# Kernel optimization log

Measured on AMD Instinct MI355X. Metric: run time of the kernel, lower is better.

## Reference

```python
import jax, jax.numpy as jnp
import numpy as np

B, T, D, H = 4, 2048, 1024, 16
HD = D // H
EPS = 1e-5


def gelu_tanh(x):
    c = jnp.sqrt(jnp.asarray(2.0 / jnp.pi, x.dtype))
    return 0.5 * x * (1.0 + jnp.tanh(c * (x + 0.044715 * x * x * x)))


def layernorm(x, gamma, beta):
    mean = jnp.mean(x, axis=-1, keepdims=True)
    var = jnp.var(x, axis=-1, keepdims=True)
    return gamma * (x - mean) / jnp.sqrt(var + EPS) + beta


def setup_inputs() -> dict:
    key = jax.random.key(0)
    ks = jax.random.split(key, 12)
    s = 0.02
    return {
        "x": jax.random.normal(ks[0], (B, T, D), jnp.float32),
        "Wq": jax.random.normal(ks[1], (D, D), jnp.float32) * s,
        "Wk": jax.random.normal(ks[2], (D, D), jnp.float32) * s,
        "Wv": jax.random.normal(ks[3], (D, D), jnp.float32) * s,
        "Wo": jax.random.normal(ks[4], (D, D), jnp.float32) * s,
        "bo": jnp.zeros((D,), jnp.float32),
        "W1": jax.random.normal(ks[5], (D, 4 * D), jnp.float32) * s,
        "b1": jnp.zeros((4 * D,), jnp.float32),
        "W2": jax.random.normal(ks[6], (4 * D, D), jnp.float32) * s,
        "b2": jnp.zeros((D,), jnp.float32),
        "gamma1": jnp.ones((D,), jnp.float32),
        "beta1": jnp.zeros((D,), jnp.float32),
        "gamma2": jnp.ones((D,), jnp.float32),
        "beta2": jnp.zeros((D,), jnp.float32),
    }


def reference(x, Wq, Wk, Wv, Wo, bo, W1, b1, W2, b2, gamma1, beta1, gamma2, beta2):
    # --- attention sublayer (pre-norm, causal) ---
    h = layernorm(x, gamma1, beta1)
    q = (h @ Wq).reshape(B, T, H, HD).transpose(0, 2, 1, 3)  # (B,H,T,hd)
    k = (h @ Wk).reshape(B, T, H, HD).transpose(0, 2, 1, 3)
    v = (h @ Wv).reshape(B, T, H, HD).transpose(0, 2, 1, 3)
    scores = jnp.einsum("bhqd,bhkd->bhqk", q, k) * (HD ** -0.5)
    causal = jnp.tril(jnp.ones((T, T), bool))
    scores = jnp.where(causal, scores, -jnp.inf)
    w = jax.nn.softmax(scores, axis=-1)
    attn = jnp.einsum("bhqk,bhkd->bhqd", w, v).transpose(0, 2, 1, 3).reshape(B, T, D)
    x = x + (attn @ Wo + bo)
    # --- FFN sublayer ---
    h2 = layernorm(x, gamma2, beta2)
    ff = gelu_tanh(h2 @ W1 + b1) @ W2 + b2
    return x + ff
```

## Files before the change

### kernel.cpp

```cpp
#include <hip/hip_runtime.h>
#include <hip/hip_bf16.h>


typedef __bf16 bf16;
typedef __attribute__((ext_vector_type(8))) __bf16 bf16x8;
typedef __attribute__((ext_vector_type(4))) __bf16 bf16x4;
typedef __attribute__((ext_vector_type(4))) float floatx4;

#define EXPC 0.18033688011112042f

__device__ __forceinline__ void async_cp16(const bf16* g, bf16* l) {
  __builtin_amdgcn_global_load_lds(
      (const __attribute__((address_space(1))) void*)g,
      (__attribute__((address_space(3))) void*)l, 16, 0, 0);
}

__global__ __launch_bounds__(256) void transpose_cvt4(
    const float* __restrict__ S0, const float* __restrict__ S1,
    const float* __restrict__ S2, const float* __restrict__ S3,
    bf16* __restrict__ D0, bf16* __restrict__ D1, bf16* __restrict__ D2,
    bf16* __restrict__ D3, int K, int N) {
  const float* W = (blockIdx.z == 0) ? S0 : (blockIdx.z == 1) ? S1
                   : (blockIdx.z == 2) ? S2 : S3;
  bf16* WT = (blockIdx.z == 0) ? D0 : (blockIdx.z == 1) ? D1
             : (blockIdx.z == 2) ? D2 : D3;
  __shared__ bf16 tile[32][33];
  const int tn = blockIdx.x;
  const int tk = blockIdx.y;
  const int t = threadIdx.x;
  const int row = t >> 3;
  const int c4 = (t & 7) * 4;

  const float* src = W + (size_t)(tk * 32 + row) * N + tn * 32 + c4;
  float4 v = *(const float4*)src;
  tile[row][c4 + 0] = (bf16)v.x;
  tile[row][c4 + 1] = (bf16)v.y;
  tile[row][c4 + 2] = (bf16)v.z;
  tile[row][c4 + 3] = (bf16)v.w;
  __syncthreads();
  bf16x4 o;
  o[0] = tile[c4 + 0][row];
  o[1] = tile[c4 + 1][row];
  o[2] = tile[c4 + 2][row];
  o[3] = tile[c4 + 3][row];
  *(bf16x4*)(WT + (size_t)(tn * 32 + row) * K + tk * 32 + c4) = o;
}

__global__ __launch_bounds__(256) void transpose_cvt(
    const float* __restrict__ W, bf16* __restrict__ WT, int K, int N) {
  __shared__ bf16 tile[32][33];
  const int tn = blockIdx.x;
  const int tk = blockIdx.y;
  const int t = threadIdx.x;
  const int row = t >> 3;
  const int c4 = (t & 7) * 4;

  const float* src = W + (size_t)(tk * 32 + row) * N + tn * 32 + c4;
  float4 v = *(const float4*)src;
  tile[row][c4 + 0] = (bf16)v.x;
  tile[row][c4 + 1] = (bf16)v.y;
  tile[row][c4 + 2] = (bf16)v.z;
  tile[row][c4 + 3] = (bf16)v.w;
  __syncthreads();
  bf16x4 o;
  o[0] = tile[c4 + 0][row];
  o[1] = tile[c4 + 1][row];
  o[2] = tile[c4 + 2][row];
  o[3] = tile[c4 + 3][row];
  *(bf16x4*)(WT + (size_t)(tn * 32 + row) * K + tk * 32 + c4) = o;
}

__global__ __launch_bounds__(256) void ln_kernel(
    const float* __restrict__ x, const float* __restrict__ gamma,
    const float* __restrict__ beta, bf16* __restrict__ out) {
  const int row = blockIdx.x;
  const int t = threadIdx.x;
  const float* xr = x + (size_t)row * 1024;
  float4 v4 = *(const float4*)(xr + t * 4);
  float a[4] = {v4.x, v4.y, v4.z, v4.w};
  float s = a[0] + a[1] + a[2] + a[3];
  float ss = a[0] * a[0] + a[1] * a[1] + a[2] * a[2] + a[3] * a[3];
  for (int off = 1; off < 64; off <<= 1) {
    s += __shfl_xor(s, off);
    ss += __shfl_xor(ss, off);
  }
  __shared__ float red[8];
  const int wid = t >> 6, lane = t & 63;
  if (lane == 0) { red[wid] = s; red[wid + 4] = ss; }
  __syncthreads();
  s = red[0] + red[1] + red[2] + red[3];
  ss = red[4] + red[5] + red[6] + red[7];
  const float mean = s * (1.0f / 1024.0f);
  const float var = ss * (1.0f / 1024.0f) - mean * mean;
  const float rstd = rsqrtf(var + 1e-5f);
  bf16x4 o;
  for (int j = 0; j < 4; ++j) {
    float g = gamma[t * 4 + j];
    float b = beta[t * 4 + j];
    o[j] = (bf16)((a[j] - mean) * rstd * g + b);
  }
  *(bf16x4*)(out + (size_t)row * 1024 + t * 4) = o;
}

__device__ __forceinline__ float gelu_f(float x) {
  const float c = 0.7978845608028654f;
  float u = c * (x + 0.044715f * x * x * x);
  u = fminf(fmaxf(u, -10.0f), 10.0f);
  float t = __builtin_exp2f(u * 2.8853900817779268f);
  return x * t * __builtin_amdgcn_rcpf(t + 1.0f);
}

template <int MODE, int BK>
__global__ __launch_bounds__(256, 2) void gemm_bt(
    const bf16* __restrict__ A, const bf16* __restrict__ BT,
    const float* __restrict__ bias, const float* __restrict__ resid,
    void* __restrict__ out, int M, int N, int K) {
  __shared__ bf16 sA[128 * BK];
  __shared__ bf16 sB[128 * BK];
  constexpr int GPR = BK / 8;
  constexpr int CPT = GPR / 2;
  constexpr int RPI = 256 / GPR;
  constexpr int SW = (BK >= 64) ? 7 : 0;

  const int t = threadIdx.x;
  const int lane = t & 63, wid = t >> 6;
  const int waveM = wid >> 1, waveN = wid & 1;
  const int quad = lane >> 4, l16 = lane & 15;
  const size_t m0 = (size_t)blockIdx.x * 128;
  const size_t n0 = (size_t)blockIdx.y * 128;

  floatx4 acc[4][4] = {};

  const int r0 = t / GPR;
  const int gp = t % GPR;
  const int gsrc = gp ^ (r0 & SW);
  const bf16* Ag = A + (m0 + r0) * (size_t)K + gsrc * 8;
  const bf16* Bg = BT + (n0 + r0) * (size_t)K + gsrc * 8;
  bf16* sAp = sA + t * 8;
  bf16* sBp = sB + t * 8;

  for (int k0 = 0; k0 < K; k0 += BK) {
    __syncthreads();
#pragma unroll
    for (int it = 0; it < CPT; ++it) {
      async_cp16(Ag + k0 + (size_t)(it * RPI) * K, sAp + it * 2048);
      async_cp16(Bg + k0 + (size_t)(it * RPI) * K, sBp + it * 2048);
    }
    __syncthreads();
#pragma unroll
    for (int ks = 0; ks < BK / 32; ++ks) {
      bf16x8 af[4], bfv[4];
#pragma unroll
      for (int i = 0; i < 4; ++i) {
        const int rowA = waveM * 64 + i * 16 + l16;
        const int g = ((ks * 4 + quad) ^ (l16 & SW)) * 8;
        af[i] = *(const bf16x8*)&sA[rowA * BK + g];
        const int rowB = waveN * 64 + i * 16 + l16;
        bfv[i] = *(const bf16x8*)&sB[rowB * BK + g];
      }
#pragma unroll
      for (int mt = 0; mt < 4; ++mt)
#pragma unroll
        for (int nt = 0; nt < 4; ++nt)
          acc[mt][nt] = __builtin_amdgcn_mfma_f32_16x16x32_bf16(
              af[mt], bfv[nt], acc[mt][nt], 0, 0, 0);
    }
  }

#pragma unroll
  for (int mt = 0; mt < 4; ++mt) {
#pragma unroll
    for (int nt = 0; nt < 4; ++nt) {
      const size_t row_base = m0 + waveM * 64 + mt * 16 + quad * 4;
      const size_t col = n0 + waveN * 64 + nt * 16 + l16;
#pragma unroll
      for (int r = 0; r < 4; ++r) {
        const size_t row = row_base + r;
        float v = acc[mt][nt][r];
        if (MODE == 1) {
          v = gelu_f(v + bias[col]);
          ((bf16*)out)[row * N + col] = (bf16)v;
        } else if (MODE == 2) {
          v += bias[col] + resid[row * N + col];
          ((float*)out)[row * N + col] = v;
        } else {
          ((bf16*)out)[row * N + col] = (bf16)v;
        }
      }
    }
  }
}

__global__ __launch_bounds__(256) void attn_kernel(
    const bf16* __restrict__ QKV, bf16* __restrict__ O) {
  const int idx = blockIdx.x;
  const int qt = 31 - (idx >> 6);
  const int bh = idx & 63;
  const int b = bh >> 4, h = bh & 15;
  const int t = threadIdx.x;
  const int lane = t & 63, wid = t >> 6;
  const int quad = lane >> 4, l16 = lane & 15;

  __shared__ bf16 sQ[64][72];
  __shared__ bf16 sK[64][72];
  __shared__ bf16 sVt[64][72];
  __shared__ bf16 sP[4][16][72];

  const size_t qbase = (size_t)b * 2048 * 3072 + (size_t)h * 64;
  const size_t kbase = qbase + 1024;
  const size_t vbase = qbase + 2048;
  const int q0 = qt * 64;

  for (int c = t; c < 512; c += 256) {
    int row = c >> 3, sub = (c & 7) * 8;
    *(bf16x8*)&sQ[row][sub] =
        *(const bf16x8*)(QKV + qbase + (size_t)(q0 + row) * 3072 + sub);
  }
  __syncthreads();

  bf16x8 aq[2];
  aq[0] = *(const bf16x8*)&sQ[wid * 16 + l16][quad * 8];
  aq[1] = *(const bf16x8*)&sQ[wid * 16 + l16][32 + quad * 8];

  float l_part[4] = {0.f, 0.f, 0.f, 0.f};
  floatx4 o_acc[4] = {};

  for (int kt = 0; kt <= qt; ++kt) {
    __syncthreads();
    const int k0 = kt * 64;
    for (int c = t; c < 512; c += 256) {
      int row = c >> 3, sub = (c & 7) * 8;
      *(bf16x8*)&sK[row][sub] =
          *(const bf16x8*)(QKV + kbase + (size_t)(k0 + row) * 3072 + sub);
      bf16x8 v8 = *(const bf16x8*)(QKV + vbase + (size_t)(k0 + row) * 3072 + sub);
#pragma unroll
      for (int j = 0; j < 8; ++j)
        sVt[sub + j][row ^ (sub & 56)] = v8[j];
    }
    __syncthreads();

    float p[4][4];
#pragma unroll
    for (int nt = 0; nt < 4; ++nt) {
      floatx4 acc = {};
#pragma unroll
      for (int ks = 0; ks < 2; ++ks) {
        bf16x8 bk = *(const bf16x8*)&sK[nt * 16 + l16][ks * 32 + quad * 8];
        acc = __builtin_amdgcn_mfma_f32_16x16x32_bf16(aq[ks], bk, acc, 0, 0, 0);
      }
#pragma unroll
      for (int r = 0; r < 4; ++r) p[nt][r] = exp2f(acc[r] * EXPC);
    }

    if (kt == qt) {
      const int qrow_base = q0 + wid * 16 + quad * 4;
#pragma unroll
      for (int nt = 0; nt < 4; ++nt) {
        const int kk = k0 + nt * 16 + l16;
#pragma unroll
        for (int r = 0; r < 4; ++r)
          if (kk > qrow_base + r) p[nt][r] = 0.f;
      }
    }

#pragma unroll
    for (int nt = 0; nt < 4; ++nt)
#pragma unroll
      for (int r = 0; r < 4; ++r) {
        l_part[r] += p[nt][r];
        sP[wid][quad * 4 + r][nt * 16 + l16] = (bf16)p[nt][r];
      }

    bf16x8 ap[2];
    ap[0] = *(const bf16x8*)&sP[wid][l16][quad * 8];
    ap[1] = *(const bf16x8*)&sP[wid][l16][32 + quad * 8];
#pragma unroll
    for (int nt = 0; nt < 4; ++nt) {
      const int r2 = nt * 16 + l16;
#pragma unroll
      for (int ks = 0; ks < 2; ++ks) {
        bf16x8 bv =
            *(const bf16x8*)&sVt[r2][(ks * 32 + quad * 8) ^ (r2 & 56)];
        o_acc[nt] =
            __builtin_amdgcn_mfma_f32_16x16x32_bf16(ap[ks], bv, o_acc[nt], 0, 0, 0);
      }
    }
  }

#pragma unroll
  for (int off = 1; off < 16; off <<= 1)
#pragma unroll
    for (int r = 0; r < 4; ++r) l_part[r] += __shfl_xor(l_part[r], off);
  float inv[4];
#pragma unroll
  for (int r = 0; r < 4; ++r) inv[r] = 1.0f / l_part[r];

#pragma unroll
  for (int nt = 0; nt < 4; ++nt)
#pragma unroll
    for (int r = 0; r < 4; ++r) {
      const size_t row = (size_t)b * 2048 + q0 + wid * 16 + quad * 4 + r;
      const size_t col = (size_t)h * 64 + nt * 16 + l16;
      O[row * 1024 + col] = (bf16)(o_acc[nt][r] * inv[r]);
    }
}

extern "C" void kernel_launch(void* const* d_in, const int* in_sizes, int n_in,
                              void* d_out, int out_size, void* d_ws, size_t ws_size,
                              hipStream_t stream) {
  const float* x = (const float*)d_in[0];
  const float* Wq = (const float*)d_in[1];
  const float* Wk = (const float*)d_in[2];
  const float* Wv = (const float*)d_in[3];
  const float* Wo = (const float*)d_in[4];
  const float* bo = (const float*)d_in[5];
  const float* W1 = (const float*)d_in[6];
  const float* b1 = (const float*)d_in[7];
  const float* W2 = (const float*)d_in[8];
  const float* b2 = (const float*)d_in[9];
  const float* gamma1 = (const float*)d_in[10];
  const float* beta1 = (const float*)d_in[11];
  const float* gamma2 = (const float*)d_in[12];
  const float* beta2 = (const float*)d_in[13];

  char* ws = (char*)d_ws;
  const size_t MB = (size_t)1 << 20;
  bf16* WqkvT = (bf16*)(ws + 0 * MB);
  bf16* WoT = (bf16*)(ws + 6 * MB);
  bf16* W1T = (bf16*)(ws + 8 * MB);
  bf16* W2T = (bf16*)(ws + 16 * MB);
  bf16* h1  = (bf16*)(ws + 24 * MB);
  bf16* QKVb = (bf16*)(ws + 40 * MB);
  bf16* attnb = (bf16*)(ws + 88 * MB);
  float* x1 = (float*)(ws + 104 * MB);
  bf16* h2  = (bf16*)(ws + 136 * MB);
  bf16* midb = (bf16*)(ws + 152 * MB);

  dim3 blk(256);

  transpose_cvt4<<<dim3(32, 32, 4), blk, 0, stream>>>(
      Wq, Wk, Wv, Wo, WqkvT, WqkvT + (size_t)1024 * 1024,
      WqkvT + (size_t)2048 * 1024, WoT, 1024, 1024);
  transpose_cvt<<<dim3(128, 32), blk, 0, stream>>>(W1, W1T, 1024, 4096);
  transpose_cvt<<<dim3(32, 128), blk, 0, stream>>>(W2, W2T, 4096, 1024);

  ln_kernel<<<8192, blk, 0, stream>>>(x, gamma1, beta1, h1);

  gemm_bt<3, 64><<<dim3(64, 24), blk, 0, stream>>>(h1, WqkvT, nullptr, nullptr,
                                                   QKVb, 8192, 3072, 1024);

  attn_kernel<<<dim3(2048), blk, 0, stream>>>(QKVb, attnb);

  gemm_bt<2, 128><<<dim3(64, 8), blk, 0, stream>>>(attnb, WoT, bo, x, x1,
                                                   8192, 1024, 1024);

  ln_kernel<<<8192, blk, 0, stream>>>(x1, gamma2, beta2, h2);

  gemm_bt<1, 64><<<dim3(64, 32), blk, 0, stream>>>(h2, W1T, b1, nullptr, midb,
                                                   8192, 4096, 1024);

  gemm_bt<2, 128><<<dim3(64, 8), blk, 0, stream>>>(midb, W2T, b2, x1, d_out,
                                                   8192, 1024, 4096);
}
```

Measured before the change: 464.3 us.

## Enlarge attention query tile to 128 rows so each K/V tile is reused

The attention kernel now handles 128 query rows per block instead of 64, with each wave computing two 16-row MFMA tiles against every staged K/V tile. This halves the number of K/V loads into shared memory per query row and halves the grid size. The K/V staging is restructured to use precomputed pointers and packed bf16x2 transposed V writes, and V fragments are loaded into registers once per tile. Costs are higher register pressure, fewer blocks for occupancy and load balance, and some wasted work on the diagonal tiles where the causal mask covers two K tiles.

```diff
diff --git a/kernel.cpp b/kernel.cpp
--- a/kernel.cpp
+++ b/kernel.cpp
@@ -5,6 +5,7 @@
 typedef __bf16 bf16;
 typedef __attribute__((ext_vector_type(8))) __bf16 bf16x8;
 typedef __attribute__((ext_vector_type(4))) __bf16 bf16x4;
+typedef __attribute__((ext_vector_type(2))) __bf16 bf16x2;
 typedef __attribute__((ext_vector_type(4))) float floatx4;
 
 #define EXPC 0.18033688011112042f
@@ -194,115 +195,147 @@
 __global__ __launch_bounds__(256) void attn_kernel(
     const bf16* __restrict__ QKV, bf16* __restrict__ O) {
   const int idx = blockIdx.x;
-  const int qt = 31 - (idx >> 6);
+  const int qt = 15 - (idx >> 6);
   const int bh = idx & 63;
   const int b = bh >> 4, h = bh & 15;
   const int t = threadIdx.x;
   const int lane = t & 63, wid = t >> 6;
   const int quad = lane >> 4, l16 = lane & 15;
 
-  __shared__ bf16 sQ[64][72];
+  __shared__ bf16 sQ[128][72];
   __shared__ bf16 sK[64][72];
   __shared__ bf16 sVt[64][72];
   __shared__ bf16 sP[4][16][72];
 
   const size_t qbase = (size_t)b * 2048 * 3072 + (size_t)h * 64;
-  const size_t kbase = qbase + 1024;
-  const size_t vbase = qbase + 2048;
-  const int q0 = qt * 64;
-
-  for (int c = t; c < 512; c += 256) {
+  const int q0 = qt * 128;
+
+  for (int c = t; c < 1024; c += 256) {
     int row = c >> 3, sub = (c & 7) * 8;
     *(bf16x8*)&sQ[row][sub] =
         *(const bf16x8*)(QKV + qbase + (size_t)(q0 + row) * 3072 + sub);
   }
   __syncthreads();
 
-  bf16x8 aq[2];
-  aq[0] = *(const bf16x8*)&sQ[wid * 16 + l16][quad * 8];
-  aq[1] = *(const bf16x8*)&sQ[wid * 16 + l16][32 + quad * 8];
-
-  float l_part[4] = {0.f, 0.f, 0.f, 0.f};
-  floatx4 o_acc[4] = {};
-
-  for (int kt = 0; kt <= qt; ++kt) {
+  bf16x8 aq[2][2];
+#pragma unroll
+  for (int mt = 0; mt < 2; ++mt)
+#pragma unroll
+    for (int ks = 0; ks < 2; ++ks)
+      aq[mt][ks] =
+          *(const bf16x8*)&sQ[wid * 32 + mt * 16 + l16][ks * 32 + quad * 8];
+
+  float l_part[2][4] = {};
+  floatx4 o_acc[2][4] = {};
+
+  const int kr = t >> 3;
+  const int sub = (t & 7) * 8;
+  const bf16* pK0 = QKV + qbase + 1024 + (size_t)kr * 3072 + sub;
+  const bf16* pK1 = pK0 + (size_t)32 * 3072;
+  const int vr = kr * 2;
+  const bf16* pV0 = QKV + qbase + 2048 + (size_t)vr * 3072 + sub;
+  const bf16* pV1 = pV0 + 3072;
+  const int vcol = vr ^ (sub & 56);
+  const ptrdiff_t bump = (ptrdiff_t)64 * 3072;
+
+  const int ktmax = 2 * qt + 1;
+  for (int kt = 0; kt <= ktmax; ++kt) {
     __syncthreads();
-    const int k0 = kt * 64;
-    for (int c = t; c < 512; c += 256) {
-      int row = c >> 3, sub = (c & 7) * 8;
-      *(bf16x8*)&sK[row][sub] =
-          *(const bf16x8*)(QKV + kbase + (size_t)(k0 + row) * 3072 + sub);
-      bf16x8 v8 = *(const bf16x8*)(QKV + vbase + (size_t)(k0 + row) * 3072 + sub);
-#pragma unroll
-      for (int j = 0; j < 8; ++j)
-        sVt[sub + j][row ^ (sub & 56)] = v8[j];
-    }
+    *(bf16x8*)&sK[kr][sub] = *(const bf16x8*)pK0;
+    *(bf16x8*)&sK[32 + kr][sub] = *(const bf16x8*)pK1;
+    bf16x8 va = *(const bf16x8*)pV0;
+    bf16x8 vb = *(const bf16x8*)pV1;
+#pragma unroll
+    for (int j = 0; j < 8; ++j) {
+      bf16x2 pk = {va[j], vb[j]};
+      *(bf16x2*)&sVt[sub + j][vcol] = pk;
+    }
+    pK0 += bump; pK1 += bump; pV0 += bump; pV1 += bump;
     __syncthreads();
 
-    float p[4][4];
-#pragma unroll
-    for (int nt = 0; nt < 4; ++nt) {
-      floatx4 acc = {};
-#pragma unroll
-      for (int ks = 0; ks < 2; ++ks) {
-        bf16x8 bk = *(const bf16x8*)&sK[nt * 16 + l16][ks * 32 + quad * 8];
-        acc = __builtin_amdgcn_mfma_f32_16x16x32_bf16(aq[ks], bk, acc, 0, 0, 0);
-      }
-#pragma unroll
-      for (int r = 0; r < 4; ++r) p[nt][r] = exp2f(acc[r] * EXPC);
-    }
-
-    if (kt == qt) {
-      const int qrow_base = q0 + wid * 16 + quad * 4;
-#pragma unroll
-      for (int nt = 0; nt < 4; ++nt) {
-        const int kk = k0 + nt * 16 + l16;
-#pragma unroll
-        for (int r = 0; r < 4; ++r)
-          if (kk > qrow_base + r) p[nt][r] = 0.f;
-      }
-    }
-
-#pragma unroll
-    for (int nt = 0; nt < 4; ++nt)
-#pragma unroll
-      for (int r = 0; r < 4; ++r) {
-        l_part[r] += p[nt][r];
-        sP[wid][quad * 4 + r][nt * 16 + l16] = (bf16)p[nt][r];
-      }
-
-    bf16x8 ap[2];
-    ap[0] = *(const bf16x8*)&sP[wid][l16][quad * 8];
-    ap[1] = *(const bf16x8*)&sP[wid][l16][32 + quad * 8];
+    bf16x8 bv[4][2];
 #pragma unroll
     for (int nt = 0; nt < 4; ++nt) {
       const int r2 = nt * 16 + l16;
 #pragma unroll
-      for (int ks = 0; ks < 2; ++ks) {
-        bf16x8 bv =
+      for (int ks = 0; ks < 2; ++ks)
+        bv[nt][ks] =
             *(const bf16x8*)&sVt[r2][(ks * 32 + quad * 8) ^ (r2 & 56)];
-        o_acc[nt] =
-            __builtin_amdgcn_mfma_f32_16x16x32_bf16(ap[ks], bv, o_acc[nt], 0, 0, 0);
-      }
-    }
-  }
-
-#pragma unroll
-  for (int off = 1; off < 16; off <<= 1)
-#pragma unroll
-    for (int r = 0; r < 4; ++r) l_part[r] += __shfl_xor(l_part[r], off);
-  float inv[4];
-#pragma unroll
-  for (int r = 0; r < 4; ++r) inv[r] = 1.0f / l_part[r];
-
-#pragma unroll
-  for (int nt = 0; nt < 4; ++nt)
-#pragma unroll
-    for (int r = 0; r < 4; ++r) {
-      const size_t row = (size_t)b * 2048 + q0 + wid * 16 + quad * 4 + r;
-      const size_t col = (size_t)h * 64 + nt * 16 + l16;
-      O[row * 1024 + col] = (bf16)(o_acc[nt][r] * inv[r]);
-    }
+    }
+
+    float p[2][4][4];
+#pragma unroll
+    for (int nt = 0; nt < 4; ++nt) {
+      const int r2 = nt * 16 + l16;
+      bf16x8 bk0 = *(const bf16x8*)&sK[r2][quad * 8];
+      bf16x8 bk1 = *(const bf16x8*)&sK[r2][32 + quad * 8];
+#pragma unroll
+      for (int mt = 0; mt < 2; ++mt) {
+        floatx4 acc = {};
+        acc = __builtin_amdgcn_mfma_f32_16x16x32_bf16(aq[mt][0], bk0, acc, 0, 0, 0);
+        acc = __builtin_amdgcn_mfma_f32_16x16x32_bf16(aq[mt][1], bk1, acc, 0, 0, 0);
+#pragma unroll
+        for (int r = 0; r < 4; ++r)
+          p[mt][nt][r] = __builtin_exp2f(acc[r] * EXPC);
+      }
+    }
+
+    if (kt >= ktmax - 1) {
+      const int k0 = kt * 64;
+#pragma unroll
+      for (int mt = 0; mt < 2; ++mt) {
+        const int qrow_base = q0 + wid * 32 + mt * 16 + quad * 4;
+#pragma unroll
+        for (int nt = 0; nt < 4; ++nt) {
+          const int kk = k0 + nt * 16 + l16;
+#pragma unroll
+          for (int r = 0; r < 4; ++r)
+            if (kk > qrow_base + r) p[mt][nt][r] = 0.f;
+        }
+      }
+    }
+
+#pragma unroll
+    for (int mt = 0; mt < 2; ++mt) {
+#pragma unroll
+      for (int nt = 0; nt < 4; ++nt)
+#pragma unroll
+        for (int r = 0; r < 4; ++r) {
+          l_part[mt][r] += p[mt][nt][r];
+          sP[wid][quad * 4 + r][nt * 16 + l16] = (bf16)p[mt][nt][r];
+        }
+      bf16x8 ap0 = *(const bf16x8*)&sP[wid][l16][quad * 8];
+      bf16x8 ap1 = *(const bf16x8*)&sP[wid][l16][32 + quad * 8];
+#pragma unroll
+      for (int nt = 0; nt < 4; ++nt) {
+        o_acc[mt][nt] = __builtin_amdgcn_mfma_f32_16x16x32_bf16(
+            ap0, bv[nt][0], o_acc[mt][nt], 0, 0, 0);
+        o_acc[mt][nt] = __builtin_amdgcn_mfma_f32_16x16x32_bf16(
+            ap1, bv[nt][1], o_acc[mt][nt], 0, 0, 0);
+      }
+    }
+  }
+
+#pragma unroll
+  for (int mt = 0; mt < 2; ++mt) {
+#pragma unroll
+    for (int off = 1; off < 16; off <<= 1)
+#pragma unroll
+      for (int r = 0; r < 4; ++r)
+        l_part[mt][r] += __shfl_xor(l_part[mt][r], off);
+    float inv[4];
+#pragma unroll
+    for (int r = 0; r < 4; ++r) inv[r] = 1.0f / l_part[mt][r];
+#pragma unroll
+    for (int nt = 0; nt < 4; ++nt)
+#pragma unroll
+      for (int r = 0; r < 4; ++r) {
+        const size_t row =
+            (size_t)b * 2048 + q0 + wid * 32 + mt * 16 + quad * 4 + r;
+        const size_t col = (size_t)h * 64 + nt * 16 + l16;
+        O[row * 1024 + col] = (bf16)(o_acc[mt][nt][r] * inv[r]);
+      }
+  }
 }
 
 extern "C" void kernel_launch(void* const* d_in, const int* in_sizes, int n_in,
@@ -349,7 +382,7 @@
   gemm_bt<3, 64><<<dim3(64, 24), blk, 0, stream>>>(h1, WqkvT, nullptr, nullptr,
                                                    QKVb, 8192, 3072, 1024);
 
-  attn_kernel<<<dim3(2048), blk, 0, stream>>>(QKVb, attnb);
+  attn_kernel<<<dim3(1024), blk, 0, stream>>>(QKVb, attnb);
 
   gemm_bt<2, 128><<<dim3(64, 8), blk, 0, stream>>>(attnb, WoT, bo, x, x1,
                                                    8192, 1024, 1024);
```

Result: no change. 468.0 us (+0.8%).
